# Kernel optimization log

Hardware: AMD Instinct MI355X
Metric: run time of the kernel (lower is better)

The kernel has to match this reference:

```python
import jax, jax.numpy as jnp
import numpy as np

N_NODES, D_IN, D_OUT, N_REL, N_EDGES = 100000, 128, 128, 8, 625000


def setup_inputs() -> dict:
    key = jax.random.key(0)
    ks = jax.random.split(key, 6)
    x = jax.random.normal(ks[0], (N_NODES, D_IN), dtype=jnp.float32)
    edge_index = jax.random.randint(ks[1], (2, N_EDGES), 0, N_NODES, dtype=jnp.int64)
    edge_type = jax.random.randint(ks[2], (N_EDGES,), 0, N_REL, dtype=jnp.int64)
    lim = (6.0 / (D_IN + D_OUT)) ** 0.5  # xavier_uniform
    rel_weight = jax.random.uniform(ks[3], (N_REL, D_IN, D_OUT), jnp.float32, -lim, lim)
    self_loop_weight = jax.random.uniform(ks[4], (D_IN, D_OUT), jnp.float32, -lim, lim)
    bias = jnp.zeros((D_OUT,), jnp.float32)
    return dict(x=x, edge_index=edge_index, edge_type=edge_type,
                rel_weight=rel_weight, self_loop_weight=self_loop_weight, bias=bias)


def reference(x, edge_index, edge_type, rel_weight, self_loop_weight, bias):
    N = x.shape[0]
    R = rel_weight.shape[0]
    src, dst = edge_index[0], edge_index[1]
    # Per-(relation, dst) in-degree == torch.bincount(dst) within each relation mask.
    seg = edge_type * N + dst  # combined (rel, dst) segment id
    deg = jax.ops.segment_sum(jnp.ones_like(src, dtype=x.dtype), seg, num_segments=R * N)
    deg = jnp.maximum(deg, 1.0)
    # Transform all node features by each relation weight once: [R, N, Do].
    xW = jnp.einsum('nd,rde->rne', x, rel_weight)
    # Gather per-edge messages already transformed by the edge's relation.
    messages = xW[edge_type, src] / deg[seg][:, None]  # [E, Do]
    out = x @ self_loop_weight + jax.ops.segment_sum(messages, dst, num_segments=N)
    return out + bias
```

## Files before the change

kernel.cpp:

```cpp
#include <hip/hip_runtime.h>

#define N_NODES 100000
#define DIM 128
#define N_REL 8
#define N_EDGES 625000
#define RN 800000
#define N_PADROWS 100032
#define SCAN_BLOCKS 98
#define SCAN_CHUNK 8192

__device__ __forceinline__ unsigned short f2bf(float f) {
    unsigned int u = __float_as_uint(f);
    u += 0x7fffu + ((u >> 16) & 1u);
    return (unsigned short)(u >> 16);
}

__device__ __forceinline__ float bf2f(unsigned short s) {
    return __uint_as_float(((unsigned int)s) << 16);
}

__global__ __launch_bounds__(256) void prep_kernel(const float* __restrict__ x,
                                                   const float* __restrict__ relw,
                                                   const float* __restrict__ selfw,
                                                   const int* __restrict__ dst,
                                                   const int* __restrict__ rel,
                                                   unsigned short* __restrict__ xb,
                                                   unsigned short* __restrict__ Wt,
                                                   int* __restrict__ degi,
                                                   int* __restrict__ rank) {
    int i = blockIdx.x * 256 + threadIdx.x;
    {
        float4 v = *(const float4*)(x + (size_t)i * 4);
        unsigned short t[4] = {f2bf(v.x), f2bf(v.y), f2bf(v.z), f2bf(v.w)};
        *(uint2*)(xb + (size_t)i * 4) = *(const uint2*)t;
    }
    if (i < 512) {
        uint4 z = {0, 0, 0, 0};
        *(uint4*)(xb + (size_t)N_NODES * DIM + i * 8) = z;
    }
    if (i < 147456) {
        int j = i & 7;
        int lane = (i >> 3) & 63;
        int t = (i >> 9) & 7;
        int ks = (i >> 12) & 3;
        int r = i >> 14;
        int m16 = lane & 15, quad = lane >> 4;
        int din = ks * 32 + quad * 8 + j;
        int dout = t * 16 + m16;
        float v = (r < 8) ? relw[(r << 14) + (din << 7) + dout] : selfw[(din << 7) + dout];
        Wt[i] = f2bf(v);
    }
    if (i < N_EDGES) {
        rank[i] = atomicAdd(&degi[rel[i] * N_NODES + dst[i]], 1);
    }
}

__global__ __launch_bounds__(256) void scan_kernel(const int* __restrict__ degi,
                                                   unsigned int* __restrict__ status,
                                                   int* __restrict__ offs) {
    __shared__ int lsum[256];
    __shared__ int lpfx;
    const int tid = threadIdx.x;
    const int b = blockIdx.x;
    const int base = b * SCAN_CHUNK + tid * 32;
    int v[32];
    int s = 0;
#pragma unroll
    for (int j = 0; j < 8; j++) {
        int idx = base + j * 4;
        int4 d = {0, 0, 0, 0};
        if (idx + 3 < RN) d = *(const int4*)(degi + idx);
        else {
            if (idx < RN) d.x = degi[idx];
            if (idx + 1 < RN) d.y = degi[idx + 1];
            if (idx + 2 < RN) d.z = degi[idx + 2];
        }
        v[j * 4] = d.x; v[j * 4 + 1] = d.y; v[j * 4 + 2] = d.z; v[j * 4 + 3] = d.w;
        s += d.x + d.y + d.z + d.w;
    }
    lsum[tid] = s;
    __syncthreads();
    for (int off = 1; off < 256; off <<= 1) {
        int p = (tid >= off) ? lsum[tid - off] : 0;
        __syncthreads();
        lsum[tid] += p;
        __syncthreads();
    }
    int thrbase = lsum[tid] - s;
    int total = lsum[255];

    if (b == 0) {
        if (tid == 0) {
            atomicExch(&status[0], 0x80000000u | (unsigned)total);
            lpfx = 0;
        }
    } else {
        if (tid == 0) atomicExch(&status[b], 0x40000000u | (unsigned)total);
        if (tid < 64) {
            int sum = 0;
            int j = b - 1;
            while (true) {
                int idx = j - tid;
                unsigned st = (idx >= 0) ? atomicAdd(&status[idx], 0u) : 0x80000000u;
                unsigned long long pball = __ballot(st & 0x80000000u);
                unsigned long long zball = __ballot(st == 0u);
                int fp = pball ? (__ffsll(pball) - 1) : 64;
                unsigned long long below = (fp >= 64) ? ~0ull : ((1ull << fp) - 1ull);
                if (zball & below) continue;
                int lim = (fp < 64) ? fp : 63;
                int val = (tid <= lim) ? (int)(st & 0x3fffffffu) : 0;
                for (int o = 32; o > 0; o >>= 1) val += __shfl_down(val, o);
                sum += __shfl(val, 0);
                if (fp < 64) break;
                j -= 64;
            }
            if (tid == 0) {
                atomicExch(&status[b], 0x80000000u | (unsigned)(sum + total));
                lpfx = sum;
            }
        }
    }
    __syncthreads();
    int run = lpfx + thrbase;
#pragma unroll
    for (int j = 0; j < 32; j++) {
        int idx = base + j;
        if (idx < RN) {
            offs[idx] = run;
            if (idx == RN - 1) offs[RN] = run + v[j];
            run += v[j];
        }
    }
}

__global__ __launch_bounds__(256) void fill_kernel(const int* __restrict__ src,
                                                   const int* __restrict__ dst,
                                                   const int* __restrict__ rel,
                                                   const int* __restrict__ rank,
                                                   const int* __restrict__ offs,
                                                   unsigned int* __restrict__ ebuf) {
    int e = blockIdx.x * 256 + threadIdx.x;
    if (e < N_EDGES) {
        int d = dst[e];
        int key = rel[e] * N_NODES + d;
        int pos = offs[key] + rank[e];
        ebuf[pos] = (unsigned int)src[e] | ((unsigned int)(d & 15) << 17);
    }
}

typedef __attribute__((ext_vector_type(8))) short frag8;
typedef __attribute__((ext_vector_type(4))) float f32x4;

__global__ __launch_bounds__(256, 4) void fused_kernel(const unsigned short* __restrict__ xb,
                                                       const unsigned short* __restrict__ Wt,
                                                       const int* __restrict__ offs2,
                                                       const unsigned int* __restrict__ ebuf,
                                                       const float* __restrict__ bias,
                                                       float* __restrict__ out) {
    __shared__ __align__(16) unsigned char ldsraw[16384];

    const int tid = threadIdx.x;
    const int wave = tid >> 6, lane = tid & 63;
    const int g = wave >> 1, h = wave & 1;
    const int m16 = lane & 15, quad = lane >> 4;
    const int dbase = blockIdx.x * 32 + g * 16;
    unsigned char* slab = ldsraw + wave * 4096;
    const unsigned int* xb32 = (const unsigned int*)xb;

    int cidx = dbase + lane;
    if (cidx > N_NODES) cidx = N_NODES;
    const int* obase = offs2 + (size_t)h * 4 * N_NODES + cidx;

    int obc = obase[0];
    int obn = obase[N_NODES];

    f32x4 acc[8];
#pragma unroll
    for (int t = 0; t < 8; t++) acc[t] = (f32x4){0.f, 0.f, 0.f, 0.f};

    int s0 = __builtin_amdgcn_readlane(obc, 0);
    int count = __builtin_amdgcn_readlane(obc, 16) - s0;
    unsigned int ewc = 0;
    if (lane < count) ewc = ebuf[s0 + lane];

    if (h == 0) {
        const unsigned short* ap = xb + (size_t)(dbase + m16) * DIM;
#pragma unroll
        for (int ks = 0; ks < 4; ks++) {
            frag8 a = *(const frag8*)(ap + ks * 32 + quad * 8);
            const frag8* bp = (const frag8*)Wt + ((8 * 4 + ks) * 8) * 64 + lane;
#pragma unroll
            for (int t = 0; t < 8; t++)
                acc[t] = __builtin_amdgcn_mfma_f32_16x16x32_bf16(a, bp[t * 64], acc[t], 0, 0, 0);
        }
    }

    unsigned int u0[16], v0[16];
    if (count > 0) {
        int cl = count; if (cl > 64) cl = 64;
#pragma unroll
        for (int k = 0; k < 16; k++) {
            int li = k; if (li >= cl) li = cl - 1;
            u0[k] = (unsigned int)__builtin_amdgcn_readlane((int)ewc, li);
            v0[k] = xb32[(size_t)(u0[k] & 0x1ffffu) * 64 + lane];
        }
    }

#pragma unroll 1
    for (int r = 0; r < 4; r++) {
        int s0n = __builtin_amdgcn_readlane(obn, 0);
        int cntn = __builtin_amdgcn_readlane(obn, 16) - s0n;
        unsigned int ewn = 0;
        if (r < 3 && lane < cntn) ewn = ebuf[s0n + lane];
        int obn2 = (r < 2) ? obase[(r + 2) * N_NODES] : 0;

        {
            uint4 z = {0, 0, 0, 0};
            *(uint4*)(slab + lane * 16) = z;
            *(uint4*)(slab + 1024 + lane * 16) = z;
            *(uint4*)(slab + 2048 + lane * 16) = z;
            *(uint4*)(slab + 3072 + lane * 16) = z;
        }

        if (count > 0) {
            float ax = 0.f, ay = 0.f;
            int cur = -1, cnt = 0;
#pragma unroll 1
            for (int b0 = 0; b0 < count; b0 += 64) {
                int cl = count - b0; if (cl > 64) cl = 64;
                unsigned int ew = ewc;
                if (b0 > 0) {
                    ew = 0;
                    if (b0 + lane < count) ew = ebuf[s0 + b0 + lane];
                }
#pragma unroll 1
                for (int i = 0; i < cl; i += 16) {
                    if (b0 + i > 0) {
#pragma unroll
                        for (int k = 0; k < 16; k++) {
                            int li = i + k; if (li >= cl) li = cl - 1;
                            u0[k] = (unsigned int)__builtin_amdgcn_readlane((int)ew, li);
                            v0[k] = xb32[(size_t)(u0[k] & 0x1ffffu) * 64 + lane];
                        }
                    }
                    int kk = cl - i; if (kk > 16) kk = 16;
#pragma unroll
                    for (int k = 0; k < 16; k++) {
                        if (k < kk) {
                            int dl = (int)((u0[k] >> 17) & 15u);
                            if (dl != cur) {
                                if (cnt > 0) {
                                    float inv = __builtin_amdgcn_rcpf((float)cnt);
                                    unsigned int p = (unsigned int)f2bf(ax * inv) |
                                                     ((unsigned int)f2bf(ay * inv) << 16);
                                    int bb = (lane >> 2) ^ cur;
                                    *(unsigned int*)(slab + cur * 256 + bb * 16 + (lane & 3) * 4) = p;
                                }
                                cur = dl; ax = 0.f; ay = 0.f; cnt = 0;
                            }
                            ax += bf2f((unsigned short)(v0[k] & 0xffffu));
                            ay += bf2f((unsigned short)(v0[k] >> 16));
                            cnt++;
                        }
                    }
                }
            }
            {
                float inv = __builtin_amdgcn_rcpf((float)cnt);
                unsigned int p = (unsigned int)f2bf(ax * inv) |
                                 ((unsigned int)f2bf(ay * inv) << 16);
                int bb = (lane >> 2) ^ cur;
                *(unsigned int*)(slab + cur * 256 + bb * 16 + (lane & 3) * 4) = p;
            }
        }

        if (r < 3 && cntn > 0) {
            int cl = cntn; if (cl > 64) cl = 64;
#pragma unroll
            for (int k = 0; k < 16; k++) {
                int li = k; if (li >= cl) li = cl - 1;
                u0[k] = (unsigned int)__builtin_amdgcn_readlane((int)ewn, li);
                v0[k] = xb32[(size_t)(u0[k] & 0x1ffffu) * 64 + lane];
            }
        }

#pragma unroll
        for (int ks = 0; ks < 4; ks++) {
            int bb = (4 * ks + quad) ^ m16;
            frag8 a = *(const frag8*)(slab + m16 * 256 + bb * 16);
            const frag8* bp = (const frag8*)Wt + (((h * 4 + r) * 4 + ks) * 8) * 64 + lane;
#pragma unroll
            for (int t = 0; t < 8; t++)
                acc[t] = __builtin_amdgcn_mfma_f32_16x16x32_bf16(a, bp[t * 64], acc[t], 0, 0, 0);
        }

        s0 = s0n; count = cntn; ewc = ewn; obn = obn2;
    }

    __syncthreads();
    unsigned char* mbuf = ldsraw + g * 8192;
    if (h == 1) {
#pragma unroll
        for (int t = 0; t < 8; t++)
            *(f32x4*)(mbuf + (t * 64 + lane) * 16) = acc[t];
    }
    __syncthreads();
    if (h == 0) {
#pragma unroll
        for (int t = 0; t < 8; t++) {
            f32x4 m = *(f32x4*)(mbuf + (t * 64 + lane) * 16);
            acc[t] += m;
        }

        float* S = (float*)mbuf;
#pragma unroll
        for (int hh = 0; hh < 2; hh++) {
#pragma unroll
            for (int tt = 0; tt < 4; tt++) {
                int t = hh * 4 + tt;
                float bc = bias[t * 16 + m16];
#pragma unroll
                for (int i = 0; i < 4; i++)
                    S[(quad * 4 + i) * 68 + tt * 16 + m16] = acc[t][i] + bc;
            }
#pragma unroll
            for (int c = 0; c < 4; c++) {
                int row16 = c * 4 + quad;
                int gr = dbase + row16;
                if (gr < N_NODES)
                    *(float4*)(out + (size_t)gr * DIM + hh * 64 + m16 * 4) =
                        *(float4*)(S + row16 * 68 + m16 * 4);
            }
        }
    }
}

extern "C" void kernel_launch(void* const* d_in, const int* in_sizes, int n_in,
                              void* d_out, int out_size, void* d_ws, size_t ws_size,
                              hipStream_t stream) {
    const float* x = (const float*)d_in[0];
    const int* edge_index = (const int*)d_in[1];
    const int* edge_type = (const int*)d_in[2];
    const float* relw = (const float*)d_in[3];
    const float* selfw = (const float*)d_in[4];
    const float* bias = (const float*)d_in[5];
    float* out = (float*)d_out;
    (void)in_sizes; (void)n_in; (void)out_size; (void)ws_size;

    char* ws = (char*)d_ws;
    size_t off = 0;
    unsigned short* xb = (unsigned short*)(ws + off); off += (size_t)N_PADROWS * DIM * 2;
    unsigned short* Wt = (unsigned short*)(ws + off); off += (size_t)9 * DIM * DIM * 2;
    int* offs2 = (int*)(ws + off); off += (size_t)(RN + 4) * 4;
    unsigned int* ebuf = (unsigned int*)(ws + off); off += (size_t)N_EDGES * 4;

    int* degi = (int*)d_out;
    unsigned int* status = (unsigned int*)(degi + RN);
    int* rank = (int*)(status + SCAN_BLOCKS + 2);

    const int* src = edge_index;
    const int* dst = edge_index + N_EDGES;

    hipMemsetAsync(degi, 0, (size_t)RN * 4 + (SCAN_BLOCKS + 2) * 4, stream);
    prep_kernel<<<12500, 256, 0, stream>>>(x, relw, selfw, dst, edge_type, xb, Wt, degi, rank);
    scan_kernel<<<SCAN_BLOCKS, 256, 0, stream>>>(degi, status, offs2);
    fill_kernel<<<(N_EDGES + 255) / 256, 256, 0, stream>>>(src, dst, edge_type, rank, offs2, ebuf);
    fused_kernel<<<N_PADROWS / 32, 256, 0, stream>>>(xb, Wt, offs2, ebuf, bias, out);
}
```

Baseline: 251.1 us.

## Merge memset, prep, scan and fill into one cooperative kernel with grid syncs

Replaces the memset, the prep kernel, the decoupled-lookback scan kernel and the fill kernel with a single cooperative persistent kernel of 1024 blocks. Grid-wide syncs separate the stages, and the scan becomes a two-level block-partials scan. The goal is to cut launch overhead and the serial lookback chain. In exchange it adds four grid barriers and grid-stride loops over the x conversion with fewer resident threads.

After: 730.7 us. 2.91x slower.

```diff
diff --git a/kernel.cpp b/kernel.cpp
--- a/kernel.cpp
+++ b/kernel.cpp
@@ -1,4 +1,7 @@
 #include <hip/hip_runtime.h>
+#include <hip/hip_cooperative_groups.h>
+
+namespace cg = cooperative_groups;
 
 #define N_NODES 100000
 #define DIM 128
@@ -6,8 +9,8 @@
 #define N_EDGES 625000
 #define RN 800000
 #define N_PADROWS 100032
-#define SCAN_BLOCKS 98
-#define SCAN_CHUNK 8192
+#define PRE_BLOCKS 1024
+#define PRE_THREADS (PRE_BLOCKS * 256)
 
 __device__ __forceinline__ unsigned short f2bf(float f) {
     unsigned int u = __float_as_uint(f);
@@ -19,128 +22,108 @@
     return __uint_as_float(((unsigned int)s) << 16);
 }
 
-__global__ __launch_bounds__(256) void prep_kernel(const float* __restrict__ x,
-                                                   const float* __restrict__ relw,
-                                                   const float* __restrict__ selfw,
-                                                   const int* __restrict__ dst,
-                                                   const int* __restrict__ rel,
-                                                   unsigned short* __restrict__ xb,
-                                                   unsigned short* __restrict__ Wt,
-                                                   int* __restrict__ degi,
-                                                   int* __restrict__ rank) {
-    int i = blockIdx.x * 256 + threadIdx.x;
-    {
-        float4 v = *(const float4*)(x + (size_t)i * 4);
+__global__ __launch_bounds__(256, 4) void pre_kernel(const float* __restrict__ x,
+                                                     const float* __restrict__ relw,
+                                                     const float* __restrict__ selfw,
+                                                     const int* __restrict__ src,
+                                                     const int* __restrict__ dst,
+                                                     const int* __restrict__ rel,
+                                                     unsigned short* __restrict__ xb,
+                                                     unsigned short* __restrict__ Wt,
+                                                     int* __restrict__ degi,
+                                                     int* __restrict__ rank,
+                                                     int* __restrict__ offs,
+                                                     unsigned int* __restrict__ ebuf,
+                                                     int* __restrict__ partials) {
+    cg::grid_group grid = cg::this_grid();
+    __shared__ int lsum[256];
+    __shared__ int gpx[256];
+    const int tid = threadIdx.x;
+    const int gtid = blockIdx.x * 256 + tid;
+
+    for (int i = gtid; i < RN / 4; i += PRE_THREADS) {
+        int4 z = {0, 0, 0, 0};
+        ((int4*)degi)[i] = z;
+    }
+    for (int i = gtid; i < 3200000; i += PRE_THREADS) {
+        float4 v = ((const float4*)x)[i];
         unsigned short t[4] = {f2bf(v.x), f2bf(v.y), f2bf(v.z), f2bf(v.w)};
         *(uint2*)(xb + (size_t)i * 4) = *(const uint2*)t;
     }
-    if (i < 512) {
+    if (gtid < 512) {
         uint4 z = {0, 0, 0, 0};
-        *(uint4*)(xb + (size_t)N_NODES * DIM + i * 8) = z;
-    }
-    if (i < 147456) {
-        int j = i & 7;
-        int lane = (i >> 3) & 63;
-        int t = (i >> 9) & 7;
-        int ks = (i >> 12) & 3;
-        int r = i >> 14;
+        *(uint4*)(xb + (size_t)N_NODES * DIM + gtid * 8) = z;
+    }
+    if (gtid < 147456) {
+        int j = gtid & 7;
+        int lane = (gtid >> 3) & 63;
+        int t = (gtid >> 9) & 7;
+        int ks = (gtid >> 12) & 3;
+        int r = gtid >> 14;
         int m16 = lane & 15, quad = lane >> 4;
         int din = ks * 32 + quad * 8 + j;
         int dout = t * 16 + m16;
         float v = (r < 8) ? relw[(r << 14) + (din << 7) + dout] : selfw[(din << 7) + dout];
-        Wt[i] = f2bf(v);
-    }
-    if (i < N_EDGES) {
-        rank[i] = atomicAdd(&degi[rel[i] * N_NODES + dst[i]], 1);
-    }
-}
-
-__global__ __launch_bounds__(256) void scan_kernel(const int* __restrict__ degi,
-                                                   unsigned int* __restrict__ status,
-                                                   int* __restrict__ offs) {
-    __shared__ int lsum[256];
-    __shared__ int lpfx;
-    const int tid = threadIdx.x;
-    const int b = blockIdx.x;
-    const int base = b * SCAN_CHUNK + tid * 32;
-    int v[32];
-    int s = 0;
-#pragma unroll
-    for (int j = 0; j < 8; j++) {
-        int idx = base + j * 4;
+        Wt[gtid] = f2bf(v);
+    }
+    grid.sync();
+
+    for (int e = gtid; e < N_EDGES; e += PRE_THREADS)
+        rank[e] = atomicAdd(&degi[rel[e] * N_NODES + dst[e]], 1);
+    grid.sync();
+
+    {
+        int base = blockIdx.x * 1024 + tid * 4;
         int4 d = {0, 0, 0, 0};
-        if (idx + 3 < RN) d = *(const int4*)(degi + idx);
+        if (base + 3 < RN) d = *(const int4*)(degi + base);
         else {
-            if (idx < RN) d.x = degi[idx];
-            if (idx + 1 < RN) d.y = degi[idx + 1];
-            if (idx + 2 < RN) d.z = degi[idx + 2];
-        }
-        v[j * 4] = d.x; v[j * 4 + 1] = d.y; v[j * 4 + 2] = d.z; v[j * 4 + 3] = d.w;
-        s += d.x + d.y + d.z + d.w;
-    }
-    lsum[tid] = s;
-    __syncthreads();
-    for (int off = 1; off < 256; off <<= 1) {
-        int p = (tid >= off) ? lsum[tid - off] : 0;
+            if (base < RN) d.x = degi[base];
+            if (base + 1 < RN) d.y = degi[base + 1];
+            if (base + 2 < RN) d.z = degi[base + 2];
+        }
+        int s = d.x + d.y + d.z + d.w;
+        lsum[tid] = s;
         __syncthreads();
-        lsum[tid] += p;
+        for (int off = 1; off < 256; off <<= 1) {
+            int p = (tid >= off) ? lsum[tid - off] : 0;
+            __syncthreads();
+            lsum[tid] += p;
+            __syncthreads();
+        }
+        int thrbase = lsum[tid] - s;
+        if (tid == 255) partials[blockIdx.x] = lsum[255];
+        grid.sync();
+
+        int q0 = partials[tid * 4], q1 = partials[tid * 4 + 1];
+        int q2 = partials[tid * 4 + 2], q3 = partials[tid * 4 + 3];
+        int qs = q0 + q1 + q2 + q3;
         __syncthreads();
-    }
-    int thrbase = lsum[tid] - s;
-    int total = lsum[255];
-
-    if (b == 0) {
-        if (tid == 0) {
-            atomicExch(&status[0], 0x80000000u | (unsigned)total);
-            lpfx = 0;
-        }
-    } else {
-        if (tid == 0) atomicExch(&status[b], 0x40000000u | (unsigned)total);
-        if (tid < 64) {
-            int sum = 0;
-            int j = b - 1;
-            while (true) {
-                int idx = j - tid;
-                unsigned st = (idx >= 0) ? atomicAdd(&status[idx], 0u) : 0x80000000u;
-                unsigned long long pball = __ballot(st & 0x80000000u);
-                unsigned long long zball = __ballot(st == 0u);
-                int fp = pball ? (__ffsll(pball) - 1) : 64;
-                unsigned long long below = (fp >= 64) ? ~0ull : ((1ull << fp) - 1ull);
-                if (zball & below) continue;
-                int lim = (fp < 64) ? fp : 63;
-                int val = (tid <= lim) ? (int)(st & 0x3fffffffu) : 0;
-                for (int o = 32; o > 0; o >>= 1) val += __shfl_down(val, o);
-                sum += __shfl(val, 0);
-                if (fp < 64) break;
-                j -= 64;
-            }
-            if (tid == 0) {
-                atomicExch(&status[b], 0x80000000u | (unsigned)(sum + total));
-                lpfx = sum;
-            }
-        }
-    }
-    __syncthreads();
-    int run = lpfx + thrbase;
-#pragma unroll
-    for (int j = 0; j < 32; j++) {
-        int idx = base + j;
-        if (idx < RN) {
-            offs[idx] = run;
-            if (idx == RN - 1) offs[RN] = run + v[j];
-            run += v[j];
-        }
-    }
-}
-
-__global__ __launch_bounds__(256) void fill_kernel(const int* __restrict__ src,
-                                                   const int* __restrict__ dst,
-                                                   const int* __restrict__ rel,
-                                                   const int* __restrict__ rank,
-                                                   const int* __restrict__ offs,
-                                                   unsigned int* __restrict__ ebuf) {
-    int e = blockIdx.x * 256 + threadIdx.x;
-    if (e < N_EDGES) {
+        lsum[tid] = qs;
+        __syncthreads();
+        for (int off = 1; off < 256; off <<= 1) {
+            int p = (tid >= off) ? lsum[tid - off] : 0;
+            __syncthreads();
+            lsum[tid] += p;
+            __syncthreads();
+        }
+        gpx[tid] = lsum[tid] - qs;
+        __syncthreads();
+        int b = blockIdx.x;
+        int bpfx = gpx[b >> 2];
+        int g4 = (b >> 2) * 4;
+        if ((b & 3) > 0) bpfx += partials[g4];
+        if ((b & 3) > 1) bpfx += partials[g4 + 1];
+        if ((b & 3) > 2) bpfx += partials[g4 + 2];
+
+        int run = bpfx + thrbase;
+        if (base < RN)     { offs[base]     = run; if (base == RN - 1)     offs[RN] = run + d.x; run += d.x; }
+        if (base + 1 < RN) { offs[base + 1] = run; if (base + 1 == RN - 1) offs[RN] = run + d.y; run += d.y; }
+        if (base + 2 < RN) { offs[base + 2] = run; if (base + 2 == RN - 1) offs[RN] = run + d.z; run += d.z; }
+        if (base + 3 < RN) { offs[base + 3] = run; if (base + 3 == RN - 1) offs[RN] = run + d.w; run += d.w; }
+    }
+    grid.sync();
+
+    for (int e = gtid; e < N_EDGES; e += PRE_THREADS) {
         int d = dst[e];
         int key = rel[e] * N_NODES + d;
         int pos = offs[key] + rank[e];
@@ -353,17 +336,18 @@
     unsigned short* Wt = (unsigned short*)(ws + off); off += (size_t)9 * DIM * DIM * 2;
     int* offs2 = (int*)(ws + off); off += (size_t)(RN + 4) * 4;
     unsigned int* ebuf = (unsigned int*)(ws + off); off += (size_t)N_EDGES * 4;
+    int* partials = (int*)(ws + off); off += (size_t)PRE_BLOCKS * 4;
 
     int* degi = (int*)d_out;
-    unsigned int* status = (unsigned int*)(degi + RN);
-    int* rank = (int*)(status + SCAN_BLOCKS + 2);
+    int* rank = degi + RN;
 
     const int* src = edge_index;
     const int* dst = edge_index + N_EDGES;
 
-    hipMemsetAsync(degi, 0, (size_t)RN * 4 + (SCAN_BLOCKS + 2) * 4, stream);
-    prep_kernel<<<12500, 256, 0, stream>>>(x, relw, selfw, dst, edge_type, xb, Wt, degi, rank);
-    scan_kernel<<<SCAN_BLOCKS, 256, 0, stream>>>(degi, status, offs2);
-    fill_kernel<<<(N_EDGES + 255) / 256, 256, 0, stream>>>(src, dst, edge_type, rank, offs2, ebuf);
+    void* args[] = {(void*)&x, (void*)&relw, (void*)&selfw, (void*)&src, (void*)&dst,
+                    (void*)&edge_type, (void*)&xb, (void*)&Wt, (void*)&degi, (void*)&rank,
+                    (void*)&offs2, (void*)&ebuf, (void*)&partials};
+    hipLaunchCooperativeKernel((void*)pre_kernel, dim3(PRE_BLOCKS), dim3(256),
+                               args, 0, stream);
     fused_kernel<<<N_PADROWS / 32, 256, 0, stream>>>(xb, Wt, offs2, ebuf, bias, out);
 }
```
